# Kernel tuning notes

Hardware: AMD Instinct MI355X
Metric: run time of the kernel (lower is better)

## Reference

```python
import jax, jax.numpy as jnp
import numpy as np

B, P, C = 64, 8732, 81
NEG_POS_RATIO = 3.0
NEG_LABEL_IDX = 0


def setup_inputs() -> dict:
    key = jax.random.key(0)
    k1, k2, k3, k4, k5 = jax.random.split(key, 5)
    confidence = jax.random.normal(k1, (B, P, C), dtype=jnp.float32)
    pred_loc = jax.random.normal(k2, (B, P, 4), dtype=jnp.float32)
    gt_bbox_loc = jax.random.normal(k3, (B, P, 4), dtype=jnp.float32)
    fg = jax.random.uniform(k4, (B, P)) < 0.03
    cls = jax.random.randint(k5, (B, P), 1, C)
    gt_class_labels = jnp.where(fg, cls, 0).astype(jnp.int32)
    return {"confidence": confidence, "pred_loc": pred_loc,
            "gt_class_labels": gt_class_labels, "gt_bbox_loc": gt_bbox_loc}


def hard_negative_mining(predicted_prob, gt_label, neg_pos_ratio):
    # predicted_prob, gt_label: (B, P)
    pos_flag = gt_label > 0
    prob = jnp.where(pos_flag, -1.0, predicted_prob)  # exclude positives from mining
    indices = jnp.argsort(-prob, axis=1)              # descending sort indices
    orders = jnp.argsort(indices, axis=1)             # rank of each prior in that sort
    num_pos = pos_flag.sum(axis=1, keepdims=True)
    num_neg = neg_pos_ratio * num_pos.astype(jnp.float32)
    neg_flag = orders.astype(jnp.float32) < num_neg
    return pos_flag, neg_flag


def reference(confidence, pred_loc, gt_class_labels, gt_bbox_loc):
    logp = jax.nn.log_softmax(confidence, axis=2)           # (B, P, C)
    # --- hard negative mining (no grad in original) ---
    neg_class_prob = -jax.lax.stop_gradient(logp)[:, :, NEG_LABEL_IDX]
    pos_flag, neg_flag = hard_negative_mining(neg_class_prob, gt_class_labels, NEG_POS_RATIO)
    sel_flag = pos_flag | neg_flag                          # (B, P)
    num_pos = pos_flag.sum(axis=1, keepdims=True).astype(jnp.float32)  # (B, 1)
    # --- masked cross entropy (mean over selected priors across whole batch) ---
    nll = -jnp.take_along_axis(logp, gt_class_labels[..., None].astype(jnp.int32), axis=2)[..., 0]
    n_sel = jnp.maximum(sel_flag.sum().astype(jnp.float32), 1.0)
    ce = jnp.sum(jnp.where(sel_flag, nll, 0.0)) / n_sel
    conf_loss = ce / num_pos                                # (B, 1), as in original
    # --- smooth L1 localization loss over positive priors ---
    d = pred_loc - gt_bbox_loc
    ad = jnp.abs(d)
    sl1 = jnp.where(ad < 1.0, 0.5 * d * d, ad - 0.5)        # (B, P, 4)
    pos_f = pos_flag[..., None].astype(sl1.dtype)
    n_matched = jnp.maximum(pos_flag.sum().astype(jnp.float32), 1.0)
    loc_huber_loss = jnp.sum(sl1 * pos_f) / n_matched
    return conf_loss, loc_huber_loss
```

## Files before the change

kernel.cpp:

```cpp
#include <hip/hip_runtime.h>
#include <cstdint>

#define BB 64
#define PP 8732
#define CC 81
#define PRB 64
#define TPB 256
#define NBX ((PP + PRB - 1) / PRB)

#define GLOBAL_AS __attribute__((address_space(1)))
#define LDS_AS __attribute__((address_space(3)))

__device__ __forceinline__ float wsum(float v) {
#pragma unroll
  for (int o = 32; o > 0; o >>= 1) v += __shfl_xor(v, o, 64);
  return v;
}
__device__ __forceinline__ int wsumi(int v) {
#pragma unroll
  for (int o = 32; o > 0; o >>= 1) v += __shfl_xor(v, o, 64);
  return v;
}

__global__ __launch_bounds__(TPB) void k_rowstats(
    const float* __restrict__ conf, const float* __restrict__ ploc,
    const int* __restrict__ label, const float* __restrict__ gloc,
    float* __restrict__ negp, int* __restrict__ part_cnt,
    float* __restrict__ part_nll, float* __restrict__ part_loc) {
  __shared__ float s_lin[PRB * CC];
  __shared__ float sh_n[4], sh_l[4];
  __shared__ int sh_c[4];

  const int b = blockIdx.y;
  const int bx = blockIdx.x;
  const int p0 = bx * PRB;
  const int np = min(PRB, PP - p0);
  const int tid = threadIdx.x;
  const size_t rowbase = (size_t)b * PP + p0;
  const size_t gbase = rowbase * CC;

  {
    const GLOBAL_AS float* g = (const GLOBAL_AS float*)(conf + gbase);
    LDS_AS float* l = (LDS_AS float*)s_lin;
    const int n4 = (np * CC) >> 2;
    for (int i = tid; i < n4; i += TPB)
      __builtin_amdgcn_global_load_lds((const GLOBAL_AS void*)(g + 4 * i),
                                       (LDS_AS void*)(l + 4 * i), 16, 0, 0);
  }

  const int p = tid >> 2, q = tid & 3;
  const bool act = (p < np);
  int lab = 0;
  float df = 0.0f;
  if (act) {
    lab = label[rowbase + p];
    const size_t idx = rowbase * 4 + tid;
    df = ploc[idx] - gloc[idx];
  }
  __syncthreads();

  float nll_acc = 0.0f, loc_acc = 0.0f;
  int cnt = 0;
  if (act) {
    const float* xr = s_lin + p * CC;
    float s = 0.0f;
    for (int c = q; c < CC; c += 4) s += __expf(xr[c]);
    s += __shfl_xor(s, 1, 64);
    s += __shfl_xor(s, 2, 64);
    const float lse = __logf(s);

    const bool pos = lab > 0;
    const float ad = fabsf(df);
    loc_acc = pos ? ((ad < 1.0f) ? 0.5f * df * df : ad - 0.5f) : 0.0f;
    if (q == 0) {
      negp[rowbase + p] = pos ? 0.0f : fmaxf(lse - xr[0], 0.0f);
      if (pos) { cnt = 1; nll_acc = lse - xr[lab]; }
    }
  }

  const float na = wsum(nll_acc);
  const float la = wsum(loc_acc);
  const int ca = wsumi(cnt);
  const int wave = tid >> 6, lane = tid & 63;
  if (lane == 0) { sh_n[wave] = na; sh_l[wave] = la; sh_c[wave] = ca; }
  __syncthreads();
  if (tid == 0) {
    float tn = 0.0f, tl = 0.0f; int tc = 0;
#pragma unroll
    for (int w = 0; w < 4; ++w) { tn += sh_n[w]; tl += sh_l[w]; tc += sh_c[w]; }
    const int slot = b * NBX + bx;
    part_cnt[slot] = tc;
    part_nll[slot] = tn;
    part_loc[slot] = tl;
  }
}

#define RREP 16
#define HSTR 257
#define TTK 1024
__global__ __launch_bounds__(TTK) void k_topk(
    const float* __restrict__ negp, const int* __restrict__ part_cnt,
    const float* __restrict__ part_nll, const float* __restrict__ part_loc,
    int* __restrict__ row_npos, float* __restrict__ row_nll,
    float* __restrict__ row_loc, float* __restrict__ row_topk) {
  __shared__ uint32_t s_v[PP];
  __shared__ int s_hist[RREP * HSTR];
  __shared__ int s_tot[256];
  __shared__ uint32_t s_pref;
  __shared__ int s_kk;
  __shared__ int s_npos;
  __shared__ float s_redn[TTK / 64], s_redl[TTK / 64], s_redf[TTK / 64];
  __shared__ int s_redc[TTK / 64];

  const int b = blockIdx.x;
  const int tid = threadIdx.x;
  const int lane = tid & 63, wave = tid >> 6;

  {
    const GLOBAL_AS float* g = (const GLOBAL_AS float*)(negp + (size_t)b * PP);
    LDS_AS uint32_t* l = (LDS_AS uint32_t*)s_v;
    for (int i = tid; i < PP / 4; i += TTK)
      __builtin_amdgcn_global_load_lds((const GLOBAL_AS void*)(g + 4 * i),
                                       (LDS_AS void*)(l + 4 * i), 16, 0, 0);
  }

  {
    int c = 0; float n = 0.0f, l = 0.0f;
    if (tid < NBX) {
      const int slot = b * NBX + tid;
      c = part_cnt[slot]; n = part_nll[slot]; l = part_loc[slot];
    }
    const int cc = wsumi(c);
    const float nn = wsum(n);
    const float ll = wsum(l);
    if (lane == 0) { s_redc[wave] = cc; s_redn[wave] = nn; s_redl[wave] = ll; }
  }
  for (int i = tid; i < RREP * HSTR; i += TTK) s_hist[i] = 0;
  __syncthreads();
  if (tid == 0) {
    int tc = 0; float tn = 0.0f, tl = 0.0f;
#pragma unroll
    for (int w = 0; w < TTK / 64; ++w) { tc += s_redc[w]; tn += s_redn[w]; tl += s_redl[w]; }
    row_npos[b] = tc; row_nll[b] = tn; row_loc[b] = tl;
    s_npos = tc;
  }
  __syncthreads();

  const int npos = s_npos;
  int K = 3 * npos;
  const int mx = PP - npos;
  if (K > mx) K = mx;
  if (K <= 0) {
    if (tid == 0) row_topk[b] = 0.0f;
    return;
  }

  if (tid == 0) { s_pref = 0u; s_kk = K; }
  __syncthreads();
  const int rep = tid & (RREP - 1);

  for (int pass = 0; pass < 4; ++pass) {
    const int sh = 24 - 8 * pass;
    const uint32_t himask = (pass == 0) ? 0u : (0xFFFFFFFFu << (sh + 8));
    const uint32_t pref = s_pref;
    for (int i = tid; i < PP; i += TTK) {
      const uint32_t u = s_v[i];
      if ((u & himask) == (pref & himask))
        atomicAdd(&s_hist[rep * HSTR + ((u >> sh) & 0xFF)], 1);
    }
    __syncthreads();
    if (tid < 256) {
      int tt = 0;
#pragma unroll
      for (int r = 0; r < RREP; ++r) tt += s_hist[r * HSTR + tid];
      s_tot[tid] = tt;
    }
    __syncthreads();
    for (int i = tid; i < RREP * HSTR; i += TTK) s_hist[i] = 0;
    if (tid < 64) {
      const int l = tid;
      const int e0 = s_tot[4 * l], e1 = s_tot[4 * l + 1];
      const int e2 = s_tot[4 * l + 2], e3 = s_tot[4 * l + 3];
      const int L = e0 + e1 + e2 + e3;
      int x = L;
#pragma unroll
      for (int o = 1; o < 64; o <<= 1) {
        const int v = __shfl_down(x, o, 64);
        if (l + o < 64) x += v;
      }
      const int T = x - L;
      const int S3 = e3 + T, S2 = e2 + S3, S1 = e1 + S2, S0 = e0 + S1;
      const int kk = s_kk;
      const uint32_t pf = s_pref;
      if (S0 >= kk && S1 < kk) { s_pref = pf | ((uint32_t)(4 * l + 0) << sh); s_kk = kk - S1; }
      if (S1 >= kk && S2 < kk) { s_pref = pf | ((uint32_t)(4 * l + 1) << sh); s_kk = kk - S2; }
      if (S2 >= kk && S3 < kk) { s_pref = pf | ((uint32_t)(4 * l + 2) << sh); s_kk = kk - S3; }
      if (S3 >= kk && T  < kk) { s_pref = pf | ((uint32_t)(4 * l + 3) << sh); s_kk = kk - T; }
    }
    __syncthreads();
  }

  const uint32_t T = s_pref;
  const int kk = s_kk;
  float local = 0.0f;
  for (int i = tid; i < PP; i += TTK) {
    const uint32_t u = s_v[i];
    if (u > T) local += __uint_as_float(u);
  }
  local = wsum(local);
  if (lane == 0) s_redf[wave] = local;
  __syncthreads();
  if (tid == 0) {
    float tot = 0.0f;
#pragma unroll
    for (int w = 0; w < TTK / 64; ++w) tot += s_redf[w];
    row_topk[b] = tot + (float)kk * __uint_as_float(T);
  }
}

__global__ void k_final(const int* __restrict__ row_npos, const float* __restrict__ row_nll,
                        const float* __restrict__ row_loc, const float* __restrict__ row_topk,
                        float* __restrict__ out) {
  const int lane = threadIdx.x;
  const int npos = row_npos[lane];
  const float nll = row_nll[lane] + row_topk[lane];
  const float loc = row_loc[lane];
  int K = 3 * npos;
  const int mx = PP - npos;
  if (K > mx) K = mx;
  const float nsel = (float)(npos + K);

  const float tot_nll = wsum(nll);
  const float tot_loc = wsum(loc);
  const float tot_pos = wsum((float)npos);
  const float tot_sel = wsum(nsel);

  const float ce = tot_nll / fmaxf(tot_sel, 1.0f);
  out[lane] = ce / (float)npos;
  if (lane == 0) out[BB] = tot_loc / fmaxf(tot_pos, 1.0f);
}

extern "C" void kernel_launch(void* const* d_in, const int* in_sizes, int n_in,
                              void* d_out, int out_size, void* d_ws, size_t ws_size,
                              hipStream_t stream) {
  const float* conf = (const float*)d_in[0];
  const float* ploc = (const float*)d_in[1];
  const int* label = (const int*)d_in[2];
  const float* gloc = (const float*)d_in[3];
  float* out = (float*)d_out;

  float* negp = (float*)d_ws;
  int* part_cnt = (int*)(negp + (size_t)BB * PP);
  float* part_nll = (float*)(part_cnt + BB * NBX);
  float* part_loc = part_nll + BB * NBX;
  int* row_npos = (int*)(part_loc + BB * NBX);
  float* row_nll = (float*)(row_npos + BB);
  float* row_loc = row_nll + BB;
  float* row_topk = row_loc + BB;

  dim3 g1(NBX, BB);
  hipLaunchKernelGGL(k_rowstats, g1, dim3(TPB), 0, stream,
                     conf, ploc, label, gloc, negp, part_cnt, part_nll, part_loc);
  hipLaunchKernelGGL(k_topk, dim3(BB), dim3(TTK), 0, stream,
                     negp, part_cnt, part_nll, part_loc,
                     row_npos, row_nll, row_loc, row_topk);
  hipLaunchKernelGGL(k_final, dim3(1), dim3(64), 0, stream,
                     row_npos, row_nll, row_loc, row_topk, out);
}
```

Before: 277.5 us.

## Persistent double-buffered rowstats blocks and fold final reduction into topk kernel

The rowstats kernel becomes a persistent grid of 12 blocks per batch row. Each block loops over strided 64-prior tiles and double-buffers the confidence tile into LDS through async global-to-LDS loads, using explicit vmcnt waits so the next tile streams in while the current one is computed. The topk kernel now reduces 12 partials per row in one wave and uses a last-block atomic counter to do the final cross-batch reduction, which removes the third kernel launch. The cost is hand-tuned waitcnt counts tied to the exact tile shape, and lower parallelism (768 blocks instead of about 8.8k) to hide memory latency.

```diff
diff --git a/kernel.cpp b/kernel.cpp
--- a/kernel.cpp
+++ b/kernel.cpp
@@ -7,10 +7,16 @@
 #define PRB 64
 #define TPB 256
 #define NBX ((PP + PRB - 1) / PRB)
+#define BPR 12
+#define NBLK (BB * BPR)
+#define NPTAIL (PP - (NBX - 1) * PRB)
 
 #define GLOBAL_AS __attribute__((address_space(1)))
 #define LDS_AS __attribute__((address_space(3)))
 
+#define WAITV(n) asm volatile("s_waitcnt vmcnt(" #n ")" ::: "memory")
+#define CFENCE() asm volatile("" ::: "memory")
+
 __device__ __forceinline__ float wsum(float v) {
 #pragma unroll
   for (int o = 32; o > 0; o >>= 1) v += __shfl_xor(v, o, 64);
@@ -20,75 +26,134 @@
 #pragma unroll
   for (int o = 32; o > 0; o >>= 1) v += __shfl_xor(v, o, 64);
   return v;
+}
+
+__device__ __forceinline__ void stage_full_t(LDS_AS float* dst,
+                                             const GLOBAL_AS float* src,
+                                             int wave, int lane) {
+  const int start = wave * 324;
+#pragma unroll
+  for (int t = 0; t < 5; ++t) {
+    const int idx = start + t * 64 + lane;
+    __builtin_amdgcn_global_load_lds((const GLOBAL_AS void*)(src + 4 * idx),
+                                     (LDS_AS void*)(dst + 4 * idx), 16, 0, 0);
+  }
+  const int idx = start + 320 + lane;
+  if (lane < 4)
+    __builtin_amdgcn_global_load_lds((const GLOBAL_AS void*)(src + 4 * idx),
+                                     (LDS_AS void*)(dst + 4 * idx), 16, 0, 0);
+}
+__device__ __forceinline__ void stage_tail_t(LDS_AS float* dst,
+                                             const GLOBAL_AS float* src,
+                                             int wave, int lane) {
+  const int start = wave * 142;
+  const int end = min(start + 142, 567);
+#pragma unroll
+  for (int t = 0; t < 2; ++t) {
+    const int idx = start + t * 64 + lane;
+    __builtin_amdgcn_global_load_lds((const GLOBAL_AS void*)(src + 4 * idx),
+                                     (LDS_AS void*)(dst + 4 * idx), 16, 0, 0);
+  }
+  const int idx = start + 128 + lane;
+  if (idx < end)
+    __builtin_amdgcn_global_load_lds((const GLOBAL_AS void*)(src + 4 * idx),
+                                     (LDS_AS void*)(dst + 4 * idx), 16, 0, 0);
+}
+__device__ __forceinline__ void stage_tile(float* dstbuf, const float* src0,
+                                           bool full, int wave, int lane) {
+  LDS_AS float* dst = (LDS_AS float*)dstbuf;
+  const GLOBAL_AS float* src = (const GLOBAL_AS float*)src0;
+  if (full) stage_full_t(dst, src, wave, lane);
+  else      stage_tail_t(dst, src, wave, lane);
 }
 
 __global__ __launch_bounds__(TPB) void k_rowstats(
     const float* __restrict__ conf, const float* __restrict__ ploc,
     const int* __restrict__ label, const float* __restrict__ gloc,
     float* __restrict__ negp, int* __restrict__ part_cnt,
-    float* __restrict__ part_nll, float* __restrict__ part_loc) {
-  __shared__ float s_lin[PRB * CC];
+    float* __restrict__ part_nll, float* __restrict__ part_loc,
+    int* __restrict__ fin_cnt) {
+  __shared__ __align__(16) float s_buf[2][PRB * CC];
   __shared__ float sh_n[4], sh_l[4];
   __shared__ int sh_c[4];
 
-  const int b = blockIdx.y;
-  const int bx = blockIdx.x;
-  const int p0 = bx * PRB;
-  const int np = min(PRB, PP - p0);
-  const int tid = threadIdx.x;
-  const size_t rowbase = (size_t)b * PP + p0;
-  const size_t gbase = rowbase * CC;
-
-  {
-    const GLOBAL_AS float* g = (const GLOBAL_AS float*)(conf + gbase);
-    LDS_AS float* l = (LDS_AS float*)s_lin;
-    const int n4 = (np * CC) >> 2;
-    for (int i = tid; i < n4; i += TPB)
-      __builtin_amdgcn_global_load_lds((const GLOBAL_AS void*)(g + 4 * i),
-                                       (LDS_AS void*)(l + 4 * i), 16, 0, 0);
-  }
-
+  const int bid = blockIdx.x;
+  const int b = bid / BPR, r = bid - b * BPR;
+  const int tid = threadIdx.x, lane = tid & 63, wave = tid >> 6;
   const int p = tid >> 2, q = tid & 3;
-  const bool act = (p < np);
-  int lab = 0;
-  float df = 0.0f;
-  if (act) {
-    lab = label[rowbase + p];
-    const size_t idx = rowbase * 4 + tid;
-    df = ploc[idx] - gloc[idx];
-  }
-  __syncthreads();
+  const int ntiles = (r <= 4) ? 12 : 11;
+
+  if (bid == 0 && tid == 0) *fin_cnt = 0;
+
+  int bx = r;
+  stage_tile(s_buf[0], conf + ((size_t)b * PP + (size_t)bx * PRB) * CC,
+             bx != NBX - 1, wave, lane);
 
   float nll_acc = 0.0f, loc_acc = 0.0f;
   int cnt = 0;
-  if (act) {
-    const float* xr = s_lin + p * CC;
-    float s = 0.0f;
-    for (int c = q; c < CC; c += 4) s += __expf(xr[c]);
-    s += __shfl_xor(s, 1, 64);
-    s += __shfl_xor(s, 2, 64);
-    const float lse = __logf(s);
-
-    const bool pos = lab > 0;
-    const float ad = fabsf(df);
-    loc_acc = pos ? ((ad < 1.0f) ? 0.5f * df * df : ad - 0.5f) : 0.0f;
-    if (q == 0) {
-      negp[rowbase + p] = pos ? 0.0f : fmaxf(lse - xr[0], 0.0f);
-      if (pos) { cnt = 1; nll_acc = lse - xr[lab]; }
-    }
+
+  for (int j = 0; j < ntiles; ++j) {
+    float* cbuf = s_buf[j & 1];
+    const int bxn = bx + BPR;
+    const bool hasn = (j + 1 < ntiles);
+    const int np = (bx == NBX - 1) ? NPTAIL : PRB;
+    const size_t rowbase = (size_t)b * PP + (size_t)bx * PRB;
+    const bool act = p < np;
+
+    int lab = 0; float pv = 0.0f, gv = 0.0f;
+    if (act) {
+      lab = label[rowbase + p];
+      const size_t i4 = rowbase * 4 + tid;
+      pv = ploc[i4]; gv = gloc[i4];
+    }
+
+    if (hasn) {
+      stage_tile(s_buf[(j + 1) & 1],
+                 conf + ((size_t)b * PP + (size_t)bxn * PRB) * CC,
+                 bxn != NBX - 1, wave, lane);
+      if (bxn != NBX - 1) WAITV(6); else WAITV(3);
+    } else {
+      WAITV(0);
+    }
+    __builtin_amdgcn_sched_barrier(0);
+    __builtin_amdgcn_s_barrier();
+    CFENCE();
+    __builtin_amdgcn_sched_barrier(0);
+
+    if (act) {
+      const float* xr = cbuf + p * CC;
+      float s = 0.0f;
+      for (int c = q; c < CC; c += 4) s += __expf(xr[c]);
+      s += __shfl_xor(s, 1, 64);
+      s += __shfl_xor(s, 2, 64);
+      const float lse = __logf(s);
+
+      const bool pos = lab > 0;
+      const float df = pv - gv;
+      const float ad = fabsf(df);
+      if (pos) loc_acc += (ad < 1.0f) ? 0.5f * df * df : ad - 0.5f;
+      if (q == 0) {
+        negp[rowbase + p] = pos ? 0.0f : fmaxf(lse - xr[0], 0.0f);
+        if (pos) { cnt += 1; nll_acc += lse - xr[lab]; }
+      }
+    }
+
+    CFENCE();
+    __builtin_amdgcn_sched_barrier(0);
+    __builtin_amdgcn_s_barrier();
+    bx = bxn;
   }
 
   const float na = wsum(nll_acc);
   const float la = wsum(loc_acc);
   const int ca = wsumi(cnt);
-  const int wave = tid >> 6, lane = tid & 63;
   if (lane == 0) { sh_n[wave] = na; sh_l[wave] = la; sh_c[wave] = ca; }
   __syncthreads();
   if (tid == 0) {
     float tn = 0.0f, tl = 0.0f; int tc = 0;
 #pragma unroll
     for (int w = 0; w < 4; ++w) { tn += sh_n[w]; tl += sh_l[w]; tc += sh_c[w]; }
-    const int slot = b * NBX + bx;
+    const int slot = b * BPR + r;
     part_cnt[slot] = tc;
     part_nll[slot] = tn;
     part_loc[slot] = tl;
@@ -102,15 +167,16 @@
     const float* __restrict__ negp, const int* __restrict__ part_cnt,
     const float* __restrict__ part_nll, const float* __restrict__ part_loc,
     int* __restrict__ row_npos, float* __restrict__ row_nll,
-    float* __restrict__ row_loc, float* __restrict__ row_topk) {
+    float* __restrict__ row_loc, float* __restrict__ row_topk,
+    int* __restrict__ fin_cnt, float* __restrict__ out) {
   __shared__ uint32_t s_v[PP];
   __shared__ int s_hist[RREP * HSTR];
   __shared__ int s_tot[256];
   __shared__ uint32_t s_pref;
   __shared__ int s_kk;
   __shared__ int s_npos;
-  __shared__ float s_redn[TTK / 64], s_redl[TTK / 64], s_redf[TTK / 64];
-  __shared__ int s_redc[TTK / 64];
+  __shared__ int s_last;
+  __shared__ float s_redf[TTK / 64];
 
   const int b = blockIdx.x;
   const int tid = threadIdx.x;
@@ -124,120 +190,117 @@
                                        (LDS_AS void*)(l + 4 * i), 16, 0, 0);
   }
 
-  {
+  if (wave == 0) {
     int c = 0; float n = 0.0f, l = 0.0f;
-    if (tid < NBX) {
-      const int slot = b * NBX + tid;
+    if (lane < BPR) {
+      const int slot = b * BPR + lane;
       c = part_cnt[slot]; n = part_nll[slot]; l = part_loc[slot];
     }
     const int cc = wsumi(c);
     const float nn = wsum(n);
     const float ll = wsum(l);
-    if (lane == 0) { s_redc[wave] = cc; s_redn[wave] = nn; s_redl[wave] = ll; }
+    if (lane == 0) { row_npos[b] = cc; row_nll[b] = nn; row_loc[b] = ll; s_npos = cc; }
   }
   for (int i = tid; i < RREP * HSTR; i += TTK) s_hist[i] = 0;
-  __syncthreads();
-  if (tid == 0) {
-    int tc = 0; float tn = 0.0f, tl = 0.0f;
-#pragma unroll
-    for (int w = 0; w < TTK / 64; ++w) { tc += s_redc[w]; tn += s_redn[w]; tl += s_redl[w]; }
-    row_npos[b] = tc; row_nll[b] = tn; row_loc[b] = tl;
-    s_npos = tc;
-  }
   __syncthreads();
 
   const int npos = s_npos;
   int K = 3 * npos;
   const int mx = PP - npos;
   if (K > mx) K = mx;
-  if (K <= 0) {
-    if (tid == 0) row_topk[b] = 0.0f;
-    return;
-  }
-
-  if (tid == 0) { s_pref = 0u; s_kk = K; }
-  __syncthreads();
-  const int rep = tid & (RREP - 1);
-
-  for (int pass = 0; pass < 4; ++pass) {
-    const int sh = 24 - 8 * pass;
-    const uint32_t himask = (pass == 0) ? 0u : (0xFFFFFFFFu << (sh + 8));
-    const uint32_t pref = s_pref;
+
+  if (K > 0) {
+    if (tid == 0) { s_pref = 0u; s_kk = K; }
+    __syncthreads();
+    const int rep = tid & (RREP - 1);
+
+    for (int pass = 0; pass < 4; ++pass) {
+      const int sh = 24 - 8 * pass;
+      const uint32_t himask = (pass == 0) ? 0u : (0xFFFFFFFFu << (sh + 8));
+      const uint32_t pref = s_pref;
+      for (int i = tid; i < PP; i += TTK) {
+        const uint32_t u = s_v[i];
+        if ((u & himask) == (pref & himask))
+          atomicAdd(&s_hist[rep * HSTR + ((u >> sh) & 0xFF)], 1);
+      }
+      __syncthreads();
+      if (tid < 256) {
+        int tt = 0;
+#pragma unroll
+        for (int rr = 0; rr < RREP; ++rr) tt += s_hist[rr * HSTR + tid];
+        s_tot[tid] = tt;
+      }
+      __syncthreads();
+      for (int i = tid; i < RREP * HSTR; i += TTK) s_hist[i] = 0;
+      if (tid < 64) {
+        const int l = tid;
+        const int e0 = s_tot[4 * l], e1 = s_tot[4 * l + 1];
+        const int e2 = s_tot[4 * l + 2], e3 = s_tot[4 * l + 3];
+        const int L = e0 + e1 + e2 + e3;
+        int x = L;
+#pragma unroll
+        for (int o = 1; o < 64; o <<= 1) {
+          const int v = __shfl_down(x, o, 64);
+          if (l + o < 64) x += v;
+        }
+        const int T = x - L;
+        const int S3 = e3 + T, S2 = e2 + S3, S1 = e1 + S2, S0 = e0 + S1;
+        const int kk = s_kk;
+        const uint32_t pf = s_pref;
+        if (S0 >= kk && S1 < kk) { s_pref = pf | ((uint32_t)(4 * l + 0) << sh); s_kk = kk - S1; }
+        if (S1 >= kk && S2 < kk) { s_pref = pf | ((uint32_t)(4 * l + 1) << sh); s_kk = kk - S2; }
+        if (S2 >= kk && S3 < kk) { s_pref = pf | ((uint32_t)(4 * l + 2) << sh); s_kk = kk - S3; }
+        if (S3 >= kk && T  < kk) { s_pref = pf | ((uint32_t)(4 * l + 3) << sh); s_kk = kk - T; }
+      }
+      __syncthreads();
+    }
+
+    const uint32_t T = s_pref;
+    const int kk = s_kk;
+    float local = 0.0f;
     for (int i = tid; i < PP; i += TTK) {
       const uint32_t u = s_v[i];
-      if ((u & himask) == (pref & himask))
-        atomicAdd(&s_hist[rep * HSTR + ((u >> sh) & 0xFF)], 1);
-    }
+      if (u > T) local += __uint_as_float(u);
+    }
+    local = wsum(local);
+    if (lane == 0) s_redf[wave] = local;
     __syncthreads();
-    if (tid < 256) {
-      int tt = 0;
-#pragma unroll
-      for (int r = 0; r < RREP; ++r) tt += s_hist[r * HSTR + tid];
-      s_tot[tid] = tt;
-    }
-    __syncthreads();
-    for (int i = tid; i < RREP * HSTR; i += TTK) s_hist[i] = 0;
+    if (tid == 0) {
+      float tot = 0.0f;
+#pragma unroll
+      for (int w = 0; w < TTK / 64; ++w) tot += s_redf[w];
+      row_topk[b] = tot + (float)kk * __uint_as_float(T);
+    }
+  } else {
+    if (tid == 0) row_topk[b] = 0.0f;
+  }
+
+  if (tid == 0) {
+    __threadfence();
+    s_last = (atomicAdd(fin_cnt, 1) == BB - 1) ? 1 : 0;
+  }
+  __syncthreads();
+  if (s_last) {
     if (tid < 64) {
-      const int l = tid;
-      const int e0 = s_tot[4 * l], e1 = s_tot[4 * l + 1];
-      const int e2 = s_tot[4 * l + 2], e3 = s_tot[4 * l + 3];
-      const int L = e0 + e1 + e2 + e3;
-      int x = L;
-#pragma unroll
-      for (int o = 1; o < 64; o <<= 1) {
-        const int v = __shfl_down(x, o, 64);
-        if (l + o < 64) x += v;
-      }
-      const int T = x - L;
-      const int S3 = e3 + T, S2 = e2 + S3, S1 = e1 + S2, S0 = e0 + S1;
-      const int kk = s_kk;
-      const uint32_t pf = s_pref;
-      if (S0 >= kk && S1 < kk) { s_pref = pf | ((uint32_t)(4 * l + 0) << sh); s_kk = kk - S1; }
-      if (S1 >= kk && S2 < kk) { s_pref = pf | ((uint32_t)(4 * l + 1) << sh); s_kk = kk - S2; }
-      if (S2 >= kk && S3 < kk) { s_pref = pf | ((uint32_t)(4 * l + 2) << sh); s_kk = kk - S3; }
-      if (S3 >= kk && T  < kk) { s_pref = pf | ((uint32_t)(4 * l + 3) << sh); s_kk = kk - T; }
-    }
-    __syncthreads();
-  }
-
-  const uint32_t T = s_pref;
-  const int kk = s_kk;
-  float local = 0.0f;
-  for (int i = tid; i < PP; i += TTK) {
-    const uint32_t u = s_v[i];
-    if (u > T) local += __uint_as_float(u);
-  }
-  local = wsum(local);
-  if (lane == 0) s_redf[wave] = local;
-  __syncthreads();
-  if (tid == 0) {
-    float tot = 0.0f;
-#pragma unroll
-    for (int w = 0; w < TTK / 64; ++w) tot += s_redf[w];
-    row_topk[b] = tot + (float)kk * __uint_as_float(T);
-  }
-}
-
-__global__ void k_final(const int* __restrict__ row_npos, const float* __restrict__ row_nll,
-                        const float* __restrict__ row_loc, const float* __restrict__ row_topk,
-                        float* __restrict__ out) {
-  const int lane = threadIdx.x;
-  const int npos = row_npos[lane];
-  const float nll = row_nll[lane] + row_topk[lane];
-  const float loc = row_loc[lane];
-  int K = 3 * npos;
-  const int mx = PP - npos;
-  if (K > mx) K = mx;
-  const float nsel = (float)(npos + K);
-
-  const float tot_nll = wsum(nll);
-  const float tot_loc = wsum(loc);
-  const float tot_pos = wsum((float)npos);
-  const float tot_sel = wsum(nsel);
-
-  const float ce = tot_nll / fmaxf(tot_sel, 1.0f);
-  out[lane] = ce / (float)npos;
-  if (lane == 0) out[BB] = tot_loc / fmaxf(tot_pos, 1.0f);
+      __threadfence();
+      const int np_ = row_npos[tid];
+      const float nllv = row_nll[tid] + row_topk[tid];
+      const float locv = row_loc[tid];
+      int Kq = 3 * np_;
+      const int mxq = PP - np_;
+      if (Kq > mxq) Kq = mxq;
+      const float nsel = (float)(np_ + Kq);
+
+      const float tot_nll = wsum(nllv);
+      const float tot_loc = wsum(locv);
+      const float tot_pos = wsum((float)np_);
+      const float tot_sel = wsum(nsel);
+
+      const float ce = tot_nll / fmaxf(tot_sel, 1.0f);
+      out[tid] = ce / (float)np_;
+      if (tid == 0) out[BB] = tot_loc / fmaxf(tot_pos, 1.0f);
+    }
+  }
 }
 
 extern "C" void kernel_launch(void* const* d_in, const int* in_sizes, int n_in,
@@ -251,19 +314,18 @@
 
   float* negp = (float*)d_ws;
   int* part_cnt = (int*)(negp + (size_t)BB * PP);
-  float* part_nll = (float*)(part_cnt + BB * NBX);
-  float* part_loc = part_nll + BB * NBX;
-  int* row_npos = (int*)(part_loc + BB * NBX);
+  float* part_nll = (float*)(part_cnt + BB * BPR);
+  float* part_loc = part_nll + BB * BPR;
+  int* row_npos = (int*)(part_loc + BB * BPR);
   float* row_nll = (float*)(row_npos + BB);
   float* row_loc = row_nll + BB;
   float* row_topk = row_loc + BB;
-
-  dim3 g1(NBX, BB);
-  hipLaunchKernelGGL(k_rowstats, g1, dim3(TPB), 0, stream,
-                     conf, ploc, label, gloc, negp, part_cnt, part_nll, part_loc);
+  int* fin_cnt = (int*)(row_topk + BB);
+
+  hipLaunchKernelGGL(k_rowstats, dim3(NBLK), dim3(TPB), 0, stream,
+                     conf, ploc, label, gloc, negp, part_cnt, part_nll, part_loc,
+                     fin_cnt);
   hipLaunchKernelGGL(k_topk, dim3(BB), dim3(TTK), 0, stream,
                      negp, part_cnt, part_nll, part_loc,
-                     row_npos, row_nll, row_loc, row_topk);
-  hipLaunchKernelGGL(k_final, dim3(1), dim3(64), 0, stream,
-                     row_npos, row_nll, row_loc, row_topk, out);
-}
+                     row_npos, row_nll, row_loc, row_topk, fin_cnt, out);
+}
```

Result: slower. 285.8 us (+3.0%).

## Fuse rowstats, top-k and final reduction into one kernel with last-block election

Applied to the files above, without the earlier changes.

Merges the three kernels into a single kernel. The last block to finish each batch row, detected with an atomic counter, runs the radix top-k selection over that row's negatives, and the last row to finish computes the final losses. The logsumexp stage now reads confidence directly from global memory with float4 loads, each thread covering 4 interleaved float4s per prior group, instead of staging through LDS, and PRB rises to 256 priors per block. This removes the kernel-launch gaps and the separate 1024-thread top-k pass, at the cost of the radix passes running at 256 threads and reading negp from global or L2 on each pass.

```diff
diff --git a/kernel.cpp b/kernel.cpp
--- a/kernel.cpp
+++ b/kernel.cpp
@@ -4,12 +4,12 @@
 #define BB 64
 #define PP 8732
 #define CC 81
-#define PRB 64
+#define PRB 256
 #define TPB 256
 #define NBX ((PP + PRB - 1) / PRB)
-
-#define GLOBAL_AS __attribute__((address_space(1)))
-#define LDS_AS __attribute__((address_space(3)))
+#define NPTAIL (PP - (NBX - 1) * PRB)
+#define RREP 16
+#define HSTR 257
 
 __device__ __forceinline__ float wsum(float v) {
 #pragma unroll
@@ -21,223 +21,233 @@
   for (int o = 32; o > 0; o >>= 1) v += __shfl_xor(v, o, 64);
   return v;
 }
-
-__global__ __launch_bounds__(TPB) void k_rowstats(
+__device__ __forceinline__ float hub(float d) {
+  const float ad = fabsf(d);
+  return (ad < 1.f) ? 0.5f * d * d : ad - 0.5f;
+}
+
+__global__ void k_init(int* __restrict__ row_done) {
+  const int t = threadIdx.x;
+  if (t <= BB) row_done[t] = 0;
+}
+
+__global__ __launch_bounds__(TPB) void k_fused(
     const float* __restrict__ conf, const float* __restrict__ ploc,
     const int* __restrict__ label, const float* __restrict__ gloc,
     float* __restrict__ negp, int* __restrict__ part_cnt,
-    float* __restrict__ part_nll, float* __restrict__ part_loc) {
-  __shared__ float s_lin[PRB * CC];
+    float* __restrict__ part_nll, float* __restrict__ part_loc,
+    int* __restrict__ row_npos, float* __restrict__ row_nll,
+    float* __restrict__ row_loc, float* __restrict__ row_topk,
+    int* __restrict__ row_done, float* __restrict__ out) {
+  __shared__ int s_hist[RREP * HSTR];
+  __shared__ int s_tot[256];
   __shared__ float sh_n[4], sh_l[4];
   __shared__ int sh_c[4];
-
-  const int b = blockIdx.y;
-  const int bx = blockIdx.x;
-  const int p0 = bx * PRB;
-  const int np = min(PRB, PP - p0);
-  const int tid = threadIdx.x;
-  const size_t rowbase = (size_t)b * PP + p0;
-  const size_t gbase = rowbase * CC;
+  __shared__ uint32_t s_pref;
+  __shared__ int s_kk, s_npos, s_flag, s_last;
+  __shared__ float s_redf[4];
+
+  int* fin_cnt = row_done + BB;
+
+  const int b = blockIdx.y, bx = blockIdx.x;
+  const int tid = threadIdx.x, lane = tid & 63, wave = tid >> 6;
+  const int q = tid & 3;
+  const int np = (bx == NBX - 1) ? NPTAIL : PRB;
+  const size_t rowbase = (size_t)b * PP + (size_t)bx * PRB;
+  const bool gact = tid < np;
+
+  float nll_acc = 0.f, loc_acc = 0.f;
+  int cnt = 0;
+
+  if (gact) {
+    const float* chunk = conf + (rowbase + (size_t)(tid & ~3)) * CC;
+    float a[4] = {0.f, 0.f, 0.f, 0.f};
+    float x0v[4] = {0.f, 0.f, 0.f, 0.f};
+
+    auto eat = [&](int C, float x) {
+      const float ex = __expf(x);
+      const int m = C % 81;
+      if (m <= 68) {
+        a[C / 81] += ex;
+      } else {
+        const int qt = (81 - m + 3) >> 2;
+        if (q >= qt) a[C / 81 + 1] += ex; else a[C / 81] += ex;
+      }
+      if (m == 0) { if (q == 0) x0v[C / 81] = x; }
+    };
+#pragma unroll
+    for (int t = 0; t < 20; ++t) {
+      const float4 v = *(const float4*)(chunk + 4 * (q + 4 * t));
+      eat(16 * t + 0, v.x); eat(16 * t + 1, v.y);
+      eat(16 * t + 2, v.z); eat(16 * t + 3, v.w);
+    }
+    if (q == 0) {
+      const float4 v = *(const float4*)(chunk + 320);
+      a[3] += __expf(v.x) + __expf(v.y) + __expf(v.z) + __expf(v.w);
+    }
+#pragma unroll
+    for (int j = 0; j < 4; ++j) {
+      a[j] += __shfl_xor(a[j], 1, 64);
+      a[j] += __shfl_xor(a[j], 2, 64);
+    }
+
+    const size_t pr = rowbase + tid;
+    const int lab = label[pr];
+    const int lab1 = __shfl(lab, (lane & ~3) + 1, 64);
+    const int lab2 = __shfl(lab, (lane & ~3) + 2, 64);
+    const int lab3 = __shfl(lab, (lane & ~3) + 3, 64);
+    if (lab > 0) {
+      const float4 pv = *(const float4*)(ploc + pr * 4);
+      const float4 gv = *(const float4*)(gloc + pr * 4);
+      loc_acc = hub(pv.x - gv.x) + hub(pv.y - gv.y) +
+                hub(pv.z - gv.z) + hub(pv.w - gv.w);
+    }
+    if (q == 0) {
+      const float l0 = __logf(a[0]), l1 = __logf(a[1]);
+      const float l2 = __logf(a[2]), l3 = __logf(a[3]);
+      float4 npv;
+      npv.x = (lab  > 0) ? 0.f : fmaxf(l0 - x0v[0], 0.f);
+      npv.y = (lab1 > 0) ? 0.f : fmaxf(l1 - x0v[1], 0.f);
+      npv.z = (lab2 > 0) ? 0.f : fmaxf(l2 - x0v[2], 0.f);
+      npv.w = (lab3 > 0) ? 0.f : fmaxf(l3 - x0v[3], 0.f);
+      *(float4*)(negp + pr) = npv;
+      if (lab  > 0) { ++cnt; nll_acc += l0 - conf[(pr + 0) * CC + lab ]; }
+      if (lab1 > 0) { ++cnt; nll_acc += l1 - conf[(pr + 1) * CC + lab1]; }
+      if (lab2 > 0) { ++cnt; nll_acc += l2 - conf[(pr + 2) * CC + lab2]; }
+      if (lab3 > 0) { ++cnt; nll_acc += l3 - conf[(pr + 3) * CC + lab3]; }
+    }
+  }
 
   {
-    const GLOBAL_AS float* g = (const GLOBAL_AS float*)(conf + gbase);
-    LDS_AS float* l = (LDS_AS float*)s_lin;
-    const int n4 = (np * CC) >> 2;
-    for (int i = tid; i < n4; i += TPB)
-      __builtin_amdgcn_global_load_lds((const GLOBAL_AS void*)(g + 4 * i),
-                                       (LDS_AS void*)(l + 4 * i), 16, 0, 0);
-  }
-
-  const int p = tid >> 2, q = tid & 3;
-  const bool act = (p < np);
-  int lab = 0;
-  float df = 0.0f;
-  if (act) {
-    lab = label[rowbase + p];
-    const size_t idx = rowbase * 4 + tid;
-    df = ploc[idx] - gloc[idx];
-  }
-  __syncthreads();
-
-  float nll_acc = 0.0f, loc_acc = 0.0f;
-  int cnt = 0;
-  if (act) {
-    const float* xr = s_lin + p * CC;
-    float s = 0.0f;
-    for (int c = q; c < CC; c += 4) s += __expf(xr[c]);
-    s += __shfl_xor(s, 1, 64);
-    s += __shfl_xor(s, 2, 64);
-    const float lse = __logf(s);
-
-    const bool pos = lab > 0;
-    const float ad = fabsf(df);
-    loc_acc = pos ? ((ad < 1.0f) ? 0.5f * df * df : ad - 0.5f) : 0.0f;
-    if (q == 0) {
-      negp[rowbase + p] = pos ? 0.0f : fmaxf(lse - xr[0], 0.0f);
-      if (pos) { cnt = 1; nll_acc = lse - xr[lab]; }
-    }
-  }
-
-  const float na = wsum(nll_acc);
-  const float la = wsum(loc_acc);
-  const int ca = wsumi(cnt);
-  const int wave = tid >> 6, lane = tid & 63;
-  if (lane == 0) { sh_n[wave] = na; sh_l[wave] = la; sh_c[wave] = ca; }
+    const float na = wsum(nll_acc);
+    const float la = wsum(loc_acc);
+    const int ca = wsumi(cnt);
+    if (lane == 0) { sh_n[wave] = na; sh_l[wave] = la; sh_c[wave] = ca; }
+  }
   __syncthreads();
   if (tid == 0) {
-    float tn = 0.0f, tl = 0.0f; int tc = 0;
+    float tn = 0.f, tl = 0.f; int tc = 0;
 #pragma unroll
     for (int w = 0; w < 4; ++w) { tn += sh_n[w]; tl += sh_l[w]; tc += sh_c[w]; }
     const int slot = b * NBX + bx;
-    part_cnt[slot] = tc;
-    part_nll[slot] = tn;
-    part_loc[slot] = tl;
-  }
-}
-
-#define RREP 16
-#define HSTR 257
-#define TTK 1024
-__global__ __launch_bounds__(TTK) void k_topk(
-    const float* __restrict__ negp, const int* __restrict__ part_cnt,
-    const float* __restrict__ part_nll, const float* __restrict__ part_loc,
-    int* __restrict__ row_npos, float* __restrict__ row_nll,
-    float* __restrict__ row_loc, float* __restrict__ row_topk) {
-  __shared__ uint32_t s_v[PP];
-  __shared__ int s_hist[RREP * HSTR];
-  __shared__ int s_tot[256];
-  __shared__ uint32_t s_pref;
-  __shared__ int s_kk;
-  __shared__ int s_npos;
-  __shared__ float s_redn[TTK / 64], s_redl[TTK / 64], s_redf[TTK / 64];
-  __shared__ int s_redc[TTK / 64];
-
-  const int b = blockIdx.x;
-  const int tid = threadIdx.x;
-  const int lane = tid & 63, wave = tid >> 6;
-
-  {
-    const GLOBAL_AS float* g = (const GLOBAL_AS float*)(negp + (size_t)b * PP);
-    LDS_AS uint32_t* l = (LDS_AS uint32_t*)s_v;
-    for (int i = tid; i < PP / 4; i += TTK)
-      __builtin_amdgcn_global_load_lds((const GLOBAL_AS void*)(g + 4 * i),
-                                       (LDS_AS void*)(l + 4 * i), 16, 0, 0);
-  }
-
-  {
-    int c = 0; float n = 0.0f, l = 0.0f;
-    if (tid < NBX) {
-      const int slot = b * NBX + tid;
+    part_cnt[slot] = tc; part_nll[slot] = tn; part_loc[slot] = tl;
+  }
+  __syncthreads();
+  __threadfence();
+  __syncthreads();
+  if (tid == 0) s_flag = (atomicAdd(&row_done[b], 1) == NBX - 1) ? 1 : 0;
+  __syncthreads();
+  if (!s_flag) return;
+
+  __threadfence();
+  if (wave == 0) {
+    int c = 0; float n = 0.f, l = 0.f;
+    if (lane < NBX) {
+      const int slot = b * NBX + lane;
       c = part_cnt[slot]; n = part_nll[slot]; l = part_loc[slot];
     }
-    const int cc = wsumi(c);
-    const float nn = wsum(n);
-    const float ll = wsum(l);
-    if (lane == 0) { s_redc[wave] = cc; s_redn[wave] = nn; s_redl[wave] = ll; }
-  }
-  for (int i = tid; i < RREP * HSTR; i += TTK) s_hist[i] = 0;
-  __syncthreads();
-  if (tid == 0) {
-    int tc = 0; float tn = 0.0f, tl = 0.0f;
-#pragma unroll
-    for (int w = 0; w < TTK / 64; ++w) { tc += s_redc[w]; tn += s_redn[w]; tl += s_redl[w]; }
-    row_npos[b] = tc; row_nll[b] = tn; row_loc[b] = tl;
-    s_npos = tc;
-  }
+    c = wsumi(c); n = wsum(n); l = wsum(l);
+    if (lane == 0) { row_npos[b] = c; row_nll[b] = n; row_loc[b] = l; s_npos = c; }
+  }
+  for (int i = tid; i < RREP * HSTR; i += TPB) s_hist[i] = 0;
   __syncthreads();
 
   const int npos = s_npos;
   int K = 3 * npos;
   const int mx = PP - npos;
   if (K > mx) K = mx;
-  if (K <= 0) {
-    if (tid == 0) row_topk[b] = 0.0f;
-    return;
-  }
-
-  if (tid == 0) { s_pref = 0u; s_kk = K; }
-  __syncthreads();
-  const int rep = tid & (RREP - 1);
-
-  for (int pass = 0; pass < 4; ++pass) {
-    const int sh = 24 - 8 * pass;
-    const uint32_t himask = (pass == 0) ? 0u : (0xFFFFFFFFu << (sh + 8));
-    const uint32_t pref = s_pref;
-    for (int i = tid; i < PP; i += TTK) {
-      const uint32_t u = s_v[i];
-      if ((u & himask) == (pref & himask))
-        atomicAdd(&s_hist[rep * HSTR + ((u >> sh) & 0xFF)], 1);
-    }
+  const float* vrow = negp + (size_t)b * PP;
+
+  if (K > 0) {
+    if (tid == 0) { s_pref = 0u; s_kk = K; }
     __syncthreads();
-    if (tid < 256) {
-      int tt = 0;
-#pragma unroll
-      for (int r = 0; r < RREP; ++r) tt += s_hist[r * HSTR + tid];
-      s_tot[tid] = tt;
-    }
+    const int rep = tid & (RREP - 1);
+
+    for (int pass = 0; pass < 4; ++pass) {
+      const int sh = 24 - 8 * pass;
+      const uint32_t himask = (pass == 0) ? 0u : (0xFFFFFFFFu << (sh + 8));
+      const uint32_t pref = s_pref;
+      for (int i = tid; i < PP; i += TPB) {
+        const uint32_t u = __float_as_uint(vrow[i]);
+        if ((u & himask) == (pref & himask))
+          atomicAdd(&s_hist[rep * HSTR + ((u >> sh) & 0xFF)], 1);
+      }
+      __syncthreads();
+      {
+        int tt = 0;
+#pragma unroll
+        for (int r = 0; r < RREP; ++r) tt += s_hist[r * HSTR + tid];
+        s_tot[tid] = tt;
+      }
+      __syncthreads();
+      for (int i = tid; i < RREP * HSTR; i += TPB) s_hist[i] = 0;
+      if (tid < 64) {
+        const int l = tid;
+        const int e0 = s_tot[4 * l], e1 = s_tot[4 * l + 1];
+        const int e2 = s_tot[4 * l + 2], e3 = s_tot[4 * l + 3];
+        const int L = e0 + e1 + e2 + e3;
+        int x = L;
+#pragma unroll
+        for (int o = 1; o < 64; o <<= 1) {
+          const int v = __shfl_down(x, o, 64);
+          if (l + o < 64) x += v;
+        }
+        const int T = x - L;
+        const int S3 = e3 + T, S2 = e2 + S3, S1 = e1 + S2, S0 = e0 + S1;
+        const int kk = s_kk;
+        const uint32_t pf = s_pref;
+        if (S0 >= kk && S1 < kk) { s_pref = pf | ((uint32_t)(4 * l + 0) << sh); s_kk = kk - S1; }
+        if (S1 >= kk && S2 < kk) { s_pref = pf | ((uint32_t)(4 * l + 1) << sh); s_kk = kk - S2; }
+        if (S2 >= kk && S3 < kk) { s_pref = pf | ((uint32_t)(4 * l + 2) << sh); s_kk = kk - S3; }
+        if (S3 >= kk && T  < kk) { s_pref = pf | ((uint32_t)(4 * l + 3) << sh); s_kk = kk - T; }
+      }
+      __syncthreads();
+    }
+
+    const uint32_t T = s_pref;
+    const int kk = s_kk;
+    float local = 0.f;
+    for (int i = tid; i < PP; i += TPB) {
+      const uint32_t u = __float_as_uint(vrow[i]);
+      if (u > T) local += __uint_as_float(u);
+    }
+    local = wsum(local);
+    if (lane == 0) s_redf[wave] = local;
     __syncthreads();
-    for (int i = tid; i < RREP * HSTR; i += TTK) s_hist[i] = 0;
-    if (tid < 64) {
-      const int l = tid;
-      const int e0 = s_tot[4 * l], e1 = s_tot[4 * l + 1];
-      const int e2 = s_tot[4 * l + 2], e3 = s_tot[4 * l + 3];
-      const int L = e0 + e1 + e2 + e3;
-      int x = L;
-#pragma unroll
-      for (int o = 1; o < 64; o <<= 1) {
-        const int v = __shfl_down(x, o, 64);
-        if (l + o < 64) x += v;
-      }
-      const int T = x - L;
-      const int S3 = e3 + T, S2 = e2 + S3, S1 = e1 + S2, S0 = e0 + S1;
-      const int kk = s_kk;
-      const uint32_t pf = s_pref;
-      if (S0 >= kk && S1 < kk) { s_pref = pf | ((uint32_t)(4 * l + 0) << sh); s_kk = kk - S1; }
-      if (S1 >= kk && S2 < kk) { s_pref = pf | ((uint32_t)(4 * l + 1) << sh); s_kk = kk - S2; }
-      if (S2 >= kk && S3 < kk) { s_pref = pf | ((uint32_t)(4 * l + 2) << sh); s_kk = kk - S3; }
-      if (S3 >= kk && T  < kk) { s_pref = pf | ((uint32_t)(4 * l + 3) << sh); s_kk = kk - T; }
-    }
-    __syncthreads();
-  }
-
-  const uint32_t T = s_pref;
-  const int kk = s_kk;
-  float local = 0.0f;
-  for (int i = tid; i < PP; i += TTK) {
-    const uint32_t u = s_v[i];
-    if (u > T) local += __uint_as_float(u);
-  }
-  local = wsum(local);
-  if (lane == 0) s_redf[wave] = local;
-  __syncthreads();
+    if (tid == 0) {
+      float tot = 0.f;
+#pragma unroll
+      for (int w = 0; w < 4; ++w) tot += s_redf[w];
+      row_topk[b] = tot + (float)kk * __uint_as_float(T);
+    }
+  } else {
+    if (tid == 0) row_topk[b] = 0.f;
+  }
+
   if (tid == 0) {
-    float tot = 0.0f;
-#pragma unroll
-    for (int w = 0; w < TTK / 64; ++w) tot += s_redf[w];
-    row_topk[b] = tot + (float)kk * __uint_as_float(T);
-  }
-}
-
-__global__ void k_final(const int* __restrict__ row_npos, const float* __restrict__ row_nll,
-                        const float* __restrict__ row_loc, const float* __restrict__ row_topk,
-                        float* __restrict__ out) {
-  const int lane = threadIdx.x;
-  const int npos = row_npos[lane];
-  const float nll = row_nll[lane] + row_topk[lane];
-  const float loc = row_loc[lane];
-  int K = 3 * npos;
-  const int mx = PP - npos;
-  if (K > mx) K = mx;
-  const float nsel = (float)(npos + K);
-
-  const float tot_nll = wsum(nll);
-  const float tot_loc = wsum(loc);
-  const float tot_pos = wsum((float)npos);
-  const float tot_sel = wsum(nsel);
-
-  const float ce = tot_nll / fmaxf(tot_sel, 1.0f);
-  out[lane] = ce / (float)npos;
-  if (lane == 0) out[BB] = tot_loc / fmaxf(tot_pos, 1.0f);
+    __threadfence();
+    s_last = (atomicAdd(fin_cnt, 1) == BB - 1) ? 1 : 0;
+  }
+  __syncthreads();
+  if (s_last && tid < 64) {
+    __threadfence();
+    const int np_ = row_npos[tid];
+    const float nllv = row_nll[tid] + row_topk[tid];
+    const float locv = row_loc[tid];
+    int Kq = 3 * np_;
+    const int mxq = PP - np_;
+    if (Kq > mxq) Kq = mxq;
+    const float nsel = (float)(np_ + Kq);
+
+    const float tot_nll = wsum(nllv);
+    const float tot_loc = wsum(locv);
+    const float tot_pos = wsum((float)np_);
+    const float tot_sel = wsum(nsel);
+
+    const float ce = tot_nll / fmaxf(tot_sel, 1.0f);
+    out[tid] = ce / (float)np_;
+    if (tid == 0) out[BB] = tot_loc / fmaxf(tot_pos, 1.0f);
+  }
 }
 
 extern "C" void kernel_launch(void* const* d_in, const int* in_sizes, int n_in,
@@ -257,13 +267,10 @@
   float* row_nll = (float*)(row_npos + BB);
   float* row_loc = row_nll + BB;
   float* row_topk = row_loc + BB;
-
-  dim3 g1(NBX, BB);
-  hipLaunchKernelGGL(k_rowstats, g1, dim3(TPB), 0, stream,
-                     conf, ploc, label, gloc, negp, part_cnt, part_nll, part_loc);
-  hipLaunchKernelGGL(k_topk, dim3(BB), dim3(TTK), 0, stream,
-                     negp, part_cnt, part_nll, part_loc,
-                     row_npos, row_nll, row_loc, row_topk);
-  hipLaunchKernelGGL(k_final, dim3(1), dim3(64), 0, stream,
-                     row_npos, row_nll, row_loc, row_topk, out);
-}
+  int* row_done = (int*)(row_topk + BB);
+
+  hipLaunchKernelGGL(k_init, dim3(1), dim3(128), 0, stream, row_done);
+  hipLaunchKernelGGL(k_fused, dim3(NBX, BB), dim3(TPB), 0, stream,
+                     conf, ploc, label, gloc, negp, part_cnt, part_nll, part_loc,
+                     row_npos, row_nll, row_loc, row_topk, row_done, out);
+}
```

Result: slower. 688.5 us (+148.1%).
